# Performance work log

Hardware: AMD Instinct MI355X
Metric: run time of the kernel (lower is better)

## Reference

```python
import jax, jax.numpy as jnp
import numpy as np

HEADS = 16


def setup_inputs() -> dict:
    key = jax.random.key(0)
    k1, k2, k3, k4 = jax.random.split(key, 4)
    B, S, D = 2, 2048, 1024
    x = jax.random.normal(k1, (B, S, D), dtype=jnp.float32)
    scale = 0.02
    Wq = jax.random.normal(k2, (D, D), dtype=jnp.float32) * scale
    Wk = jax.random.normal(k3, (D, D), dtype=jnp.float32) * scale
    Wv = jax.random.normal(k4, (D, D), dtype=jnp.float32) * scale
    return {"x": x, "Wq": Wq, "Wk": Wk, "Wv": Wv}


def reference(x, Wq, Wk, Wv):
    B, S, D = x.shape
    H = HEADS
    dh = D // H
    # project and split heads: (B, S, D) -> (B, H, S, dh)
    def split_heads(t):
        return t.reshape(B, S, H, dh).transpose(0, 2, 1, 3)

    q = split_heads(x @ Wq)
    k = split_heads(x @ Wk)
    v = split_heads(x @ Wv)

    # scores: (B, H, S, S)
    scores = jnp.einsum("bhqd,bhkd->bhqk", q, k)
    causal_mask = jnp.triu(jnp.ones((S, S), dtype=bool), k=1)  # True above diagonal -> masked
    scores = jnp.where(causal_mask, -jnp.inf, scores) / jnp.sqrt(jnp.float32(dh))
    weights = jax.nn.softmax(scores, axis=-1)
    # dropout is identity at inference (eval mode)
    ctx = jnp.einsum("bhqk,bhkd->bhqd", weights, v)  # (B, H, S, dh)
    return ctx.transpose(0, 2, 1, 3).reshape(B, S, D)
```

## Files before the change

kernel.cpp:

```cpp
#include <hip/hip_runtime.h>
#include <hip/hip_bf16.h>
#include <cstdint>

#define BATCH  2
#define SEQ    2048
#define DMODEL 1024
#define NH     16
#define DH     64

typedef short bf16x8 __attribute__((ext_vector_type(8)));
typedef float f32x4  __attribute__((ext_vector_type(4)));
typedef unsigned short u16;

#define MFMA16(a, b, c) __builtin_amdgcn_mfma_f32_16x16x32_bf16((a), (b), (c), 0, 0, 0)

#define GLL(gp, lp) __builtin_amdgcn_global_load_lds( \
    (const __attribute__((address_space(1))) void*)(gp), \
    (__attribute__((address_space(3))) void*)(lp), 16, 0, 0)

#define SCL 0.18033688011112042f

#if __has_builtin(__builtin_amdgcn_exp2f)
#define EXP2(x) __builtin_amdgcn_exp2f(x)
#else
#define EXP2(x) __expf((x) * 0.69314718055994531f)
#endif

static __device__ __forceinline__ u16 f2bf(float f) {
  union { float f; unsigned int i; } u; u.f = f;
  unsigned int r = u.i + 0x7FFFu + ((u.i >> 16) & 1u);
  return (u16)(r >> 16);
}

__global__ __launch_bounds__(256) void prep_kernel(const float* __restrict__ X,
                                                   const float* __restrict__ W0,
                                                   const float* __restrict__ W1,
                                                   const float* __restrict__ W2,
                                                   u16* __restrict__ Xb,
                                                   u16* __restrict__ Wt) {
  const int wg = blockIdx.x;
  const int t = threadIdx.x;
  if (wg < 2048) {
    int idx = (wg * 256 + t) * 8;
    float4 a = *reinterpret_cast<const float4*>(X + idx);
    float4 b = *reinterpret_cast<const float4*>(X + idx + 4);
    union { bf16x8 v; u16 u[8]; } pk;
    pk.u[0]=f2bf(a.x); pk.u[1]=f2bf(a.y); pk.u[2]=f2bf(a.z); pk.u[3]=f2bf(a.w);
    pk.u[4]=f2bf(b.x); pk.u[5]=f2bf(b.y); pk.u[6]=f2bf(b.z); pk.u[7]=f2bf(b.w);
    *reinterpret_cast<bf16x8*>(Xb + idx) = pk.v;
    return;
  }
  __shared__ float T[32][33];
  const int i = wg - 2048;
  const int z = i >> 10;
  const int rem = i & 1023;
  const int k0 = (rem & 31) * 32, n0 = (rem >> 5) * 32;
  const float* W = (z == 0) ? W0 : (z == 1) ? W1 : W2;
  const float sc = (z == 0) ? SCL : 1.0f;
  u16* out = Wt + (size_t)z * DMODEL * DMODEL;
  {
    int r = t >> 3, c = (t & 7) * 4;
    float4 v = *reinterpret_cast<const float4*>(W + (size_t)(k0 + r) * DMODEL + n0 + c);
    T[r][c] = v.x; T[r][c+1] = v.y; T[r][c+2] = v.z; T[r][c+3] = v.w;
  }
  __syncthreads();
  {
    int n = t >> 3, k = (t & 7) * 4;
    union { unsigned long long ll; u16 u[4]; } pk;
    pk.u[0] = f2bf(T[k][n] * sc);   pk.u[1] = f2bf(T[k+1][n] * sc);
    pk.u[2] = f2bf(T[k+2][n] * sc); pk.u[3] = f2bf(T[k+3][n] * sc);
    *reinterpret_cast<unsigned long long*>(out + (size_t)(n0 + n) * DMODEL + k0 + k) = pk.ll;
  }
}

__global__ __launch_bounds__(256) void qkv_mfma_kernel(const u16* __restrict__ Xb,
                                                       const u16* __restrict__ Wt,
                                                       u16* __restrict__ Y) {
  __shared__ u16 As[128 * 64];
  __shared__ u16 Bs[128 * 64];
  char* Ab = (char*)As; char* Bb = (char*)Bs;
  const int t = threadIdx.x;
  const int lane = t & 63;
  const int w = t >> 6;
  const int wr = w >> 1, wc = w & 1;
  const int l15 = lane & 15, lg = lane >> 4;
  const int row0 = blockIdx.x * 128;
  const int col0 = blockIdx.y * 128;
  const int z = blockIdx.z;
  const u16* Wz = Wt + (size_t)z * DMODEL * DMODEL;
  u16* Yz = Y + (size_t)z * ((size_t)BATCH * SEQ * DMODEL);

  f32x4 acc[4][4];
  #pragma unroll
  for (int mt = 0; mt < 4; ++mt)
    #pragma unroll
    for (int nt = 0; nt < 4; ++nt)
      acc[mt][nt] = (f32x4){0.f, 0.f, 0.f, 0.f};

  size_t aofs[4], bofs[4];
  #pragma unroll
  for (int it = 0; it < 4; ++it) {
    int row = it * 32 + (t >> 3);
    int sl  = (t & 7) ^ (row & 7);
    aofs[it] = (size_t)(row0 + row) * DMODEL + sl * 8;
    bofs[it] = (size_t)(col0 + row) * DMODEL + sl * 8;
  }

  for (int k0 = 0; k0 < DMODEL; k0 += 64) {
    __syncthreads();
    #pragma unroll
    for (int it = 0; it < 4; ++it) {
      GLL(Xb + aofs[it] + k0, Ab + it * 4096 + w * 1024);
      GLL(Wz + bofs[it] + k0, Bb + it * 4096 + w * 1024);
    }
    __syncthreads();
    #pragma unroll
    for (int c = 0; c < 2; ++c) {
      bf16x8 am[4], bn[4];
      int kof = c * 64 + lg * 16;
      #pragma unroll
      for (int mt = 0; mt < 4; ++mt) {
        int row = wr * 64 + mt * 16 + l15;
        am[mt] = *reinterpret_cast<const bf16x8*>(Ab + row * 128 + (kof ^ ((row & 7) << 4)));
      }
      #pragma unroll
      for (int nt = 0; nt < 4; ++nt) {
        int row = wc * 64 + nt * 16 + l15;
        bn[nt] = *reinterpret_cast<const bf16x8*>(Bb + row * 128 + (kof ^ ((row & 7) << 4)));
      }
      #pragma unroll
      for (int mt = 0; mt < 4; ++mt)
        #pragma unroll
        for (int nt = 0; nt < 4; ++nt)
          acc[mt][nt] = MFMA16(am[mt], bn[nt], acc[mt][nt]);
    }
  }

  #pragma unroll
  for (int mt = 0; mt < 4; ++mt) {
    #pragma unroll
    for (int i = 0; i < 4; ++i) {
      int bs = row0 + wr * 64 + mt * 16 + lg * 4 + i;
      int b = bs >> 11, s = bs & (SEQ - 1);
      #pragma unroll
      for (int nt = 0; nt < 4; ++nt) {
        int d = col0 + wc * 64 + nt * 16 + l15;
        int h = d >> 6, dd = d & (DH - 1);
        size_t off = (((size_t)b * NH + h) * SEQ + s) * DH + dd;
        Yz[off] = f2bf(acc[mt][nt][i]);
      }
    }
  }
}

__global__ __launch_bounds__(256) void transpose_v_kernel(const u16* __restrict__ V,
                                                          u16* __restrict__ Vt) {
  __shared__ u16 L[64][72];
  const int sb = blockIdx.x, h = blockIdx.y, b = blockIdx.z;
  const size_t hin  = ((size_t)b * NH + h) * (size_t)SEQ * DH;
  const size_t hout = ((size_t)b * NH + h) * (size_t)DH * SEQ;
  const int s0 = sb * 64;
  const int t = threadIdx.x;
  const int r = t >> 3, c = t & 7;
  #pragma unroll
  for (int it = 0; it < 2; ++it) {
    int row = r + it * 32;
    bf16x8 v = *reinterpret_cast<const bf16x8*>(V + hin + (size_t)(s0 + row) * DH + c * 8);
    *reinterpret_cast<bf16x8*>(&L[row][c * 8]) = v;
  }
  __syncthreads();
  #pragma unroll
  for (int it = 0; it < 2; ++it) {
    int d = r + it * 32;
    union { bf16x8 v; u16 u[8]; } pk;
    #pragma unroll
    for (int j = 0; j < 8; ++j) pk.u[j] = L[c * 8 + j][d];
    *reinterpret_cast<bf16x8*>(Vt + hout + (size_t)d * SEQ + s0 + c * 8) = pk.v;
  }
}

#define STAGE_KV(kb)                                                  \
  {                                                                   \
    const u16* kp_ = Kw + hq + (size_t)(kb) * (128 * DH);             \
    const u16* vp_ = Vt + hv + (size_t)(kb) * 128;                    \
    char* kd_ = (char*)Ks + dstb;                                     \
    char* vd_ = (char*)Vs + dstb;                                     \
    GLL(kp_ + kofs[0], kd_);        GLL(vp_ + vofs[0], vd_);          \
    GLL(kp_ + kofs[1], kd_ + 1024); GLL(vp_ + vofs[1], vd_ + 1024);   \
    GLL(kp_ + kofs[2], kd_ + 2048); GLL(vp_ + vofs[2], vd_ + 2048);   \
    GLL(kp_ + kofs[3], kd_ + 3072); GLL(vp_ + vofs[3], vd_ + 3072);   \
  }

__global__ __launch_bounds__(256) void flash_mfma13_kernel(const u16* __restrict__ Qw,
                                                           const u16* __restrict__ Kw,
                                                           const u16* __restrict__ Vt,
                                                           float* __restrict__ Out) {
  __shared__ u16 Ks[128 * 64];
  __shared__ u16 Vs[64 * 128];
  __shared__ u16 Pl[4][16 * 128];
  const int wgid = blockIdx.x;
  const int g = wgid & 31;
  const int qt = 31 - (wgid >> 5);
  const int b = g >> 4, h = g & 15;
  const int t = threadIdx.x, lane = t & 63, w = t >> 6;
  const int l15 = lane & 15, lg = lane >> 4;
  char* Pb = (char*)Pl[w];
  const size_t hq = ((size_t)b * NH + h) * (size_t)SEQ * DH;
  const size_t hv = ((size_t)b * NH + h) * (size_t)DH * SEQ;

  size_t kofs[4], vofs[4];
  #pragma unroll
  for (int it = 0; it < 4; ++it) {
    int i = (w * 4 + it) * 64 + lane;
    kofs[it] = (size_t)(i >> 3) * DH + (size_t)((((i & 7) ^ ((i >> 3) & 7))) * 8);
    vofs[it] = (size_t)(i >> 4) * SEQ + (size_t)((((i & 15) ^ ((i >> 4) & 7))) * 8);
  }
  const int dstb = w * 4096;

  const int csel = (l15 & 4) << 4;
  const int sw45 = (lg * 16) ^ ((l15 & 3) << 4);
  const int kb0  = l15 * 128 + sw45 + csel;
  const int kb1  = kb0 ^ 64;
  const int vbA  = l15 * 256 + sw45 + csel;
  const int vbB  = vbA ^ 64;
  const int pw0  = l15 * 256 + ((lg * 8) ^ ((l15 & 1) << 4));
  const int xw   = ((l15 >> 1) & 3) << 5;

  const int q0 = qt * 64;
  const int nkv = (qt >> 1) + 1;
  const int qrow = q0 + w * 16 + l15;

  bf16x8 qf0, qf1;
  {
    const u16* qp = Qw + hq + (size_t)qrow * DH + lg * 8;
    qf0 = *reinterpret_cast<const bf16x8*>(qp);
    qf1 = *reinterpret_cast<const bf16x8*>(qp + 32);
  }

  f32x4 o[4];
  #pragma unroll
  for (int dt = 0; dt < 4; ++dt) o[dt] = (f32x4){0.f, 0.f, 0.f, 0.f};
  float l_ = 0.f;

  #pragma unroll 1
  for (int kb = 0; kb < nkv - 1; ++kb) {
    __syncthreads();
    STAGE_KV(kb);
    __syncthreads();

    float s[8][4];
    __builtin_amdgcn_s_setprio(1);
    #pragma unroll
    for (int kt = 0; kt < 8; ++kt) {
      f32x4 sa = (f32x4){0.f, 0.f, 0.f, 0.f};
      bf16x8 kf0 = *reinterpret_cast<const bf16x8*>((char*)Ks + kb0 + kt * 2048);
      bf16x8 kf1 = *reinterpret_cast<const bf16x8*>((char*)Ks + kb1 + kt * 2048);
      sa = MFMA16(kf0, qf0, sa);
      sa = MFMA16(kf1, qf1, sa);
      #pragma unroll
      for (int i = 0; i < 4; ++i) s[kt][i] = sa[i];
    }
    __builtin_amdgcn_s_setprio(0);

    #pragma unroll
    for (int kt = 0; kt < 8; ++kt) {
      union { unsigned long long ll; __hip_bfloat16 bf[4]; } pk;
      #pragma unroll
      for (int i = 0; i < 4; ++i) {
        float e = EXP2(s[kt][i]);
        l_ += e;
        pk.bf[i] = __float2bfloat16(e);
      }
      *reinterpret_cast<unsigned long long*>(Pb + pw0 + ((kt * 32) ^ xw)) = pk.ll;
    }

    __builtin_amdgcn_s_setprio(1);
    {
      bf16x8 pa0 = *reinterpret_cast<const bf16x8*>(Pb + vbA);
      bf16x8 pa1 = *reinterpret_cast<const bf16x8*>(Pb + vbB);
      bf16x8 pa2 = *reinterpret_cast<const bf16x8*>(Pb + vbA + 128);
      bf16x8 pa3 = *reinterpret_cast<const bf16x8*>(Pb + vbB + 128);
      #pragma unroll
      for (int dt = 0; dt < 4; ++dt) {
        bf16x8 v0 = *reinterpret_cast<const bf16x8*>((char*)Vs + vbA + dt * 4096);
        bf16x8 v1 = *reinterpret_cast<const bf16x8*>((char*)Vs + vbB + dt * 4096);
        bf16x8 v2 = *reinterpret_cast<const bf16x8*>((char*)Vs + vbA + 128 + dt * 4096);
        bf16x8 v3 = *reinterpret_cast<const bf16x8*>((char*)Vs + vbB + 128 + dt * 4096);
        o[dt] = MFMA16(pa0, v0, o[dt]);
        o[dt] = MFMA16(pa1, v1, o[dt]);
        o[dt] = MFMA16(pa2, v2, o[dt]);
        o[dt] = MFMA16(pa3, v3, o[dt]);
      }
    }
    __builtin_amdgcn_s_setprio(0);
  }

  {
    const int kb = nkv - 1;
    const int k0 = kb * 128;
    __syncthreads();
    STAGE_KV(kb);
    __syncthreads();

    const int qmax = q0 + w * 16 + 15;
    const int ktlim = ((qmax - k0) >> 4) + 1;
    const int kcmax = (ktlim + 1) >> 1;

    float s[8][4];
    #pragma unroll
    for (int kt = 0; kt < 8; ++kt) {
      if (kt < ktlim) {
        f32x4 sa = (f32x4){0.f, 0.f, 0.f, 0.f};
        bf16x8 kf0 = *reinterpret_cast<const bf16x8*>((char*)Ks + kb0 + kt * 2048);
        bf16x8 kf1 = *reinterpret_cast<const bf16x8*>((char*)Ks + kb1 + kt * 2048);
        sa = MFMA16(kf0, qf0, sa);
        sa = MFMA16(kf1, qf1, sa);
        #pragma unroll
        for (int i = 0; i < 4; ++i) {
          int key = k0 + kt * 16 + lg * 4 + i;
          s[kt][i] = (key > qrow) ? -1e30f : sa[i];
        }
      } else {
        s[kt][0] = -1e30f; s[kt][1] = -1e30f; s[kt][2] = -1e30f; s[kt][3] = -1e30f;
      }
    }

    #pragma unroll
    for (int kt = 0; kt < 8; ++kt) {
      union { unsigned long long ll; __hip_bfloat16 bf[4]; } pk;
      #pragma unroll
      for (int i = 0; i < 4; ++i) {
        float e = EXP2(s[kt][i]);
        l_ += e;
        pk.bf[i] = __float2bfloat16(e);
      }
      *reinterpret_cast<unsigned long long*>(Pb + pw0 + ((kt * 32) ^ xw)) = pk.ll;
    }

    bf16x8 paq[4];
    paq[0] = *reinterpret_cast<const bf16x8*>(Pb + vbA);
    paq[1] = *reinterpret_cast<const bf16x8*>(Pb + vbB);
    paq[2] = *reinterpret_cast<const bf16x8*>(Pb + vbA + 128);
    paq[3] = *reinterpret_cast<const bf16x8*>(Pb + vbB + 128);
    #pragma unroll
    for (int kc = 0; kc < 4; ++kc) {
      if (kc >= kcmax) break;
      const int vo = (kc & 1) ? (vbB - vbA) : 0;
      const int hi = (kc >> 1) * 128;
      #pragma unroll
      for (int dt = 0; dt < 4; ++dt) {
        bf16x8 vbf = *reinterpret_cast<const bf16x8*>((char*)Vs + vbA + vo + hi + dt * 4096);
        o[dt] = MFMA16(paq[kc], vbf, o[dt]);
      }
    }
  }

  l_ += __shfl_xor(l_, 16);
  l_ += __shfl_xor(l_, 32);
  #pragma unroll
  for (int i = 0; i < 4; ++i) {
    float li = __shfl(l_, (lane & 48) + lg * 4 + i);
    float inv = 1.f / li;
    int q = q0 + w * 16 + lg * 4 + i;
    float* op = Out + ((size_t)b * SEQ + q) * DMODEL + h * DH + l15;
    #pragma unroll
    for (int dt = 0; dt < 4; ++dt) op[dt * 16] = o[dt][i] * inv;
  }
}

extern "C" void kernel_launch(void* const* d_in, const int* in_sizes, int n_in,
                              void* d_out, int out_size, void* d_ws, size_t ws_size,
                              hipStream_t stream) {
  const float* x  = (const float*)d_in[0];
  const float* Wq = (const float*)d_in[1];
  const float* Wk = (const float*)d_in[2];
  const float* Wv = (const float*)d_in[3];
  float* out = (float*)d_out;

  u16* ws  = (u16*)d_ws;
  u16* qkv = ws;
  u16* xb  = ws + 12582912;
  u16* wt  = ws + 16777216;
  u16* vt  = ws + 19922944;

  prep_kernel<<<5120, 256, 0, stream>>>(x, Wq, Wk, Wv, xb, wt);
  qkv_mfma_kernel<<<dim3(32, 8, 3), 256, 0, stream>>>(xb, wt, qkv);
  transpose_v_kernel<<<dim3(32, NH, BATCH), 256, 0, stream>>>(qkv + 8388608, vt);
  flash_mfma13_kernel<<<1024, 256, 0, stream>>>(qkv, qkv + 4194304, vt, out);
}
```

Baseline: 79.33 us.

## Shrink KV tile to 64 keys and interleave query-tile scheduling order

The flash attention kernel now stages 64-key K/V blocks instead of 128, which shrinks LDS use and the per-iteration S and P tiles. It also drops the masked-out half block on the diagonal, since query tiles are 64 rows. Workgroups are assigned query tiles in a serpentine order within groups of eight, replacing the reverse-linear order, to balance causal work across CUs. The cost is twice as many loop iterations, with more barriers and staging overhead per unit of work.

```diff
diff --git a/kernel.cpp b/kernel.cpp
--- a/kernel.cpp
+++ b/kernel.cpp
@@ -181,53 +181,55 @@
 
 #define STAGE_KV(kb)                                                  \
   {                                                                   \
-    const u16* kp_ = Kw + hq + (size_t)(kb) * (128 * DH);             \
-    const u16* vp_ = Vt + hv + (size_t)(kb) * 128;                    \
+    const u16* kp_ = Kw + hq + (size_t)(kb) * (64 * DH);              \
+    const u16* vp_ = Vt + hv + (size_t)(kb) * 64;                     \
     char* kd_ = (char*)Ks + dstb;                                     \
     char* vd_ = (char*)Vs + dstb;                                     \
-    GLL(kp_ + kofs[0], kd_);        GLL(vp_ + vofs[0], vd_);          \
-    GLL(kp_ + kofs[1], kd_ + 1024); GLL(vp_ + vofs[1], vd_ + 1024);   \
-    GLL(kp_ + kofs[2], kd_ + 2048); GLL(vp_ + vofs[2], vd_ + 2048);   \
-    GLL(kp_ + kofs[3], kd_ + 3072); GLL(vp_ + vofs[3], vd_ + 3072);   \
-  }
-
-__global__ __launch_bounds__(256) void flash_mfma13_kernel(const u16* __restrict__ Qw,
+    GLL(kp_ + kofs0, kd_);        GLL(vp_ + vofs0, vd_);              \
+    GLL(kp_ + kofs1, kd_ + 1024); GLL(vp_ + vofs1, vd_ + 1024);       \
+  }
+
+__global__ __launch_bounds__(256) void flash_mfma14_kernel(const u16* __restrict__ Qw,
                                                            const u16* __restrict__ Kw,
                                                            const u16* __restrict__ Vt,
                                                            float* __restrict__ Out) {
-  __shared__ u16 Ks[128 * 64];
-  __shared__ u16 Vs[64 * 128];
-  __shared__ u16 Pl[4][16 * 128];
+  __shared__ u16 Ks[64 * 64];
+  __shared__ u16 Vs[64 * 64];
+  __shared__ u16 Pl[4][16 * 64];
   const int wgid = blockIdx.x;
   const int g = wgid & 31;
-  const int qt = 31 - (wgid >> 5);
+  const int j = (wgid >> 5) & 7;
+  const int r = wgid >> 8;
+  const int qt = r * 8 + ((r & 1) ? (7 - j) : j);
   const int b = g >> 4, h = g & 15;
+  const int nkv = qt + 1;
+
   const int t = threadIdx.x, lane = t & 63, w = t >> 6;
   const int l15 = lane & 15, lg = lane >> 4;
   char* Pb = (char*)Pl[w];
   const size_t hq = ((size_t)b * NH + h) * (size_t)SEQ * DH;
   const size_t hv = ((size_t)b * NH + h) * (size_t)DH * SEQ;
 
-  size_t kofs[4], vofs[4];
-  #pragma unroll
-  for (int it = 0; it < 4; ++it) {
-    int i = (w * 4 + it) * 64 + lane;
-    kofs[it] = (size_t)(i >> 3) * DH + (size_t)((((i & 7) ^ ((i >> 3) & 7))) * 8);
-    vofs[it] = (size_t)(i >> 4) * SEQ + (size_t)((((i & 15) ^ ((i >> 4) & 7))) * 8);
-  }
-  const int dstb = w * 4096;
+  int kofs0, kofs1, vofs0, vofs1;
+  {
+    int i0 = (w * 2 + 0) * 64 + lane, i1 = (w * 2 + 1) * 64 + lane;
+    int r0 = i0 >> 3, s0 = i0 & 7;
+    int r1 = i1 >> 3, s1 = i1 & 7;
+    kofs0 = r0 * DH  + ((s0 ^ (r0 & 7)) * 8);
+    kofs1 = r1 * DH  + ((s1 ^ (r1 & 7)) * 8);
+    vofs0 = r0 * SEQ + ((s0 ^ (r0 & 7)) * 8);
+    vofs1 = r1 * SEQ + ((s1 ^ (r1 & 7)) * 8);
+  }
+  const int dstb = w * 2048;
 
   const int csel = (l15 & 4) << 4;
   const int sw45 = (lg * 16) ^ ((l15 & 3) << 4);
-  const int kb0  = l15 * 128 + sw45 + csel;
-  const int kb1  = kb0 ^ 64;
-  const int vbA  = l15 * 256 + sw45 + csel;
-  const int vbB  = vbA ^ 64;
-  const int pw0  = l15 * 256 + ((lg * 8) ^ ((l15 & 1) << 4));
+  const int rb0  = l15 * 128 + sw45 + csel;
+  const int rb1  = rb0 ^ 64;
+  const int pw0  = l15 * 128 + ((lg * 8) ^ ((l15 & 1) << 4));
   const int xw   = ((l15 >> 1) & 3) << 5;
 
   const int q0 = qt * 64;
-  const int nkv = (qt >> 1) + 1;
   const int qrow = q0 + w * 16 + l15;
 
   bf16x8 qf0, qf1;
@@ -248,13 +250,13 @@
     STAGE_KV(kb);
     __syncthreads();
 
-    float s[8][4];
+    float s[4][4];
     __builtin_amdgcn_s_setprio(1);
     #pragma unroll
-    for (int kt = 0; kt < 8; ++kt) {
+    for (int kt = 0; kt < 4; ++kt) {
       f32x4 sa = (f32x4){0.f, 0.f, 0.f, 0.f};
-      bf16x8 kf0 = *reinterpret_cast<const bf16x8*>((char*)Ks + kb0 + kt * 2048);
-      bf16x8 kf1 = *reinterpret_cast<const bf16x8*>((char*)Ks + kb1 + kt * 2048);
+      bf16x8 kf0 = *reinterpret_cast<const bf16x8*>((char*)Ks + rb0 + kt * 2048);
+      bf16x8 kf1 = *reinterpret_cast<const bf16x8*>((char*)Ks + rb1 + kt * 2048);
       sa = MFMA16(kf0, qf0, sa);
       sa = MFMA16(kf1, qf1, sa);
       #pragma unroll
@@ -263,7 +265,7 @@
     __builtin_amdgcn_s_setprio(0);
 
     #pragma unroll
-    for (int kt = 0; kt < 8; ++kt) {
+    for (int kt = 0; kt < 4; ++kt) {
       union { unsigned long long ll; __hip_bfloat16 bf[4]; } pk;
       #pragma unroll
       for (int i = 0; i < 4; ++i) {
@@ -276,20 +278,14 @@
 
     __builtin_amdgcn_s_setprio(1);
     {
-      bf16x8 pa0 = *reinterpret_cast<const bf16x8*>(Pb + vbA);
-      bf16x8 pa1 = *reinterpret_cast<const bf16x8*>(Pb + vbB);
-      bf16x8 pa2 = *reinterpret_cast<const bf16x8*>(Pb + vbA + 128);
-      bf16x8 pa3 = *reinterpret_cast<const bf16x8*>(Pb + vbB + 128);
+      bf16x8 pa0 = *reinterpret_cast<const bf16x8*>(Pb + rb0);
+      bf16x8 pa1 = *reinterpret_cast<const bf16x8*>(Pb + rb1);
       #pragma unroll
       for (int dt = 0; dt < 4; ++dt) {
-        bf16x8 v0 = *reinterpret_cast<const bf16x8*>((char*)Vs + vbA + dt * 4096);
-        bf16x8 v1 = *reinterpret_cast<const bf16x8*>((char*)Vs + vbB + dt * 4096);
-        bf16x8 v2 = *reinterpret_cast<const bf16x8*>((char*)Vs + vbA + 128 + dt * 4096);
-        bf16x8 v3 = *reinterpret_cast<const bf16x8*>((char*)Vs + vbB + 128 + dt * 4096);
+        bf16x8 v0 = *reinterpret_cast<const bf16x8*>((char*)Vs + rb0 + dt * 2048);
+        bf16x8 v1 = *reinterpret_cast<const bf16x8*>((char*)Vs + rb1 + dt * 2048);
         o[dt] = MFMA16(pa0, v0, o[dt]);
         o[dt] = MFMA16(pa1, v1, o[dt]);
-        o[dt] = MFMA16(pa2, v2, o[dt]);
-        o[dt] = MFMA16(pa3, v3, o[dt]);
       }
     }
     __builtin_amdgcn_s_setprio(0);
@@ -297,22 +293,21 @@
 
   {
     const int kb = nkv - 1;
-    const int k0 = kb * 128;
+    const int k0 = kb * 64;
     __syncthreads();
     STAGE_KV(kb);
     __syncthreads();
 
-    const int qmax = q0 + w * 16 + 15;
-    const int ktlim = ((qmax - k0) >> 4) + 1;
-    const int kcmax = (ktlim + 1) >> 1;
-
-    float s[8][4];
-    #pragma unroll
-    for (int kt = 0; kt < 8; ++kt) {
+    const int ktlim = w + 1;
+    const int kcmax = (w + 2) >> 1;
+
+    float s[4][4];
+    #pragma unroll
+    for (int kt = 0; kt < 4; ++kt) {
       if (kt < ktlim) {
         f32x4 sa = (f32x4){0.f, 0.f, 0.f, 0.f};
-        bf16x8 kf0 = *reinterpret_cast<const bf16x8*>((char*)Ks + kb0 + kt * 2048);
-        bf16x8 kf1 = *reinterpret_cast<const bf16x8*>((char*)Ks + kb1 + kt * 2048);
+        bf16x8 kf0 = *reinterpret_cast<const bf16x8*>((char*)Ks + rb0 + kt * 2048);
+        bf16x8 kf1 = *reinterpret_cast<const bf16x8*>((char*)Ks + rb1 + kt * 2048);
         sa = MFMA16(kf0, qf0, sa);
         sa = MFMA16(kf1, qf1, sa);
         #pragma unroll
@@ -326,7 +321,7 @@
     }
 
     #pragma unroll
-    for (int kt = 0; kt < 8; ++kt) {
+    for (int kt = 0; kt < 4; ++kt) {
       union { unsigned long long ll; __hip_bfloat16 bf[4]; } pk;
       #pragma unroll
       for (int i = 0; i < 4; ++i) {
@@ -337,20 +332,16 @@
       *reinterpret_cast<unsigned long long*>(Pb + pw0 + ((kt * 32) ^ xw)) = pk.ll;
     }
 
-    bf16x8 paq[4];
-    paq[0] = *reinterpret_cast<const bf16x8*>(Pb + vbA);
-    paq[1] = *reinterpret_cast<const bf16x8*>(Pb + vbB);
-    paq[2] = *reinterpret_cast<const bf16x8*>(Pb + vbA + 128);
-    paq[3] = *reinterpret_cast<const bf16x8*>(Pb + vbB + 128);
-    #pragma unroll
-    for (int kc = 0; kc < 4; ++kc) {
+    bf16x8 pa0 = *reinterpret_cast<const bf16x8*>(Pb + rb0);
+    bf16x8 pa1 = *reinterpret_cast<const bf16x8*>(Pb + rb1);
+    #pragma unroll
+    for (int kc = 0; kc < 2; ++kc) {
       if (kc >= kcmax) break;
-      const int vo = (kc & 1) ? (vbB - vbA) : 0;
-      const int hi = (kc >> 1) * 128;
+      const int off = kc ? (rb1 - rb0) : 0;
       #pragma unroll
       for (int dt = 0; dt < 4; ++dt) {
-        bf16x8 vbf = *reinterpret_cast<const bf16x8*>((char*)Vs + vbA + vo + hi + dt * 4096);
-        o[dt] = MFMA16(paq[kc], vbf, o[dt]);
+        bf16x8 vv = *reinterpret_cast<const bf16x8*>((char*)Vs + rb0 + off + dt * 2048);
+        o[dt] = MFMA16(kc ? pa1 : pa0, vv, o[dt]);
       }
     }
   }
@@ -386,5 +377,5 @@
   prep_kernel<<<5120, 256, 0, stream>>>(x, Wq, Wk, Wv, xb, wt);
   qkv_mfma_kernel<<<dim3(32, 8, 3), 256, 0, stream>>>(xb, wt, qkv);
   transpose_v_kernel<<<dim3(32, NH, BATCH), 256, 0, stream>>>(qkv + 8388608, vt);
-  flash_mfma13_kernel<<<1024, 256, 0, stream>>>(qkv, qkv + 4194304, vt, out);
-}
+  flash_mfma14_kernel<<<1024, 256, 0, stream>>>(qkv, qkv + 4194304, vt, out);
+}
```

Result: slower. 81.85 us (+3.2%).
